# Kernel tuning notes

Measured on AMD Instinct MI355X. Metric: run time of the kernel, lower is better.

Reference implementation:

```python
import jax, jax.numpy as jnp
import numpy as np
from jax import lax


def grouped_linear(x, w):
    # x: [d0, d1, G*ws], w: [G, ws, out_per_group] -> [d0, d1, G*out_per_group]
    d0, d1, _ = x.shape
    G, ws, o = w.shape
    x = x.reshape(d0, d1, G, ws)
    return jnp.einsum('btgi,gio->btgh'.replace('h', 'o'), x, w).reshape(d0, d1, G * o)


def gru_layer(x, w_ih, w_hh, b_ih, b_hh):
    # x: [T, H_in]; w_ih/w_hh: [3, H, H_in]; b_ih/b_hh: [3, H]; gate order (r, z, n)
    ih = jnp.einsum('ti,ghi->tgh', x, w_ih) + b_ih  # input projections for all t at once

    def step(h, ih_t):
        hh = jnp.einsum('i,ghi->gh', h, w_hh) + b_hh
        r = jax.nn.sigmoid(ih_t[0] + hh[0])
        z = jax.nn.sigmoid(ih_t[1] + hh[1])
        n = jnp.tanh(ih_t[2] + r * hh[2])
        h_new = n + z * (h - n)
        return h_new, h_new

    h0 = jnp.zeros((w_hh.shape[1],), x.dtype)
    _, ys = lax.scan(step, h0, ih)
    return ys  # [T, H]


def setup_inputs() -> dict:
    key = jax.random.key(0)
    T, B, H = 8192, 1, 512
    HID, G, L = 512, 8, 2
    C_IN, C_OUT, F, KT = 64, 10, 96, 2
    ks = jax.random.split(key, 17)
    s = jnp.float32(0.05)
    return {
        'emb_tbh': jax.random.normal(ks[0], (T, B, H), jnp.float32),
        'c0': jax.random.normal(ks[1], (B, C_IN, T, F), jnp.float32),
        'lin_in_w': jax.random.normal(ks[2], (G, H // G, HID // G), jnp.float32) * s,
        'gru_w_ih': jax.random.normal(ks[3], (L, 3, HID, HID), jnp.float32) * s,
        'gru_w_hh': jax.random.normal(ks[4], (L, 3, HID, HID), jnp.float32) * s,
        'gru_b_ih': jax.random.normal(ks[5], (L, 3, HID), jnp.float32) * s,
        'gru_b_hh': jax.random.normal(ks[6], (L, 3, HID), jnp.float32) * s,
        'gru_skip_w': jax.random.normal(ks[7], (HID, HID), jnp.float32) * s,
        'gru_skip_b': jax.random.normal(ks[8], (HID,), jnp.float32) * s,
        'lin_out_w': jax.random.normal(ks[9], (G, HID // G, HID // G), jnp.float32) * s,
        'df_skip_w': jax.random.normal(ks[10], (HID, H), jnp.float32) * s,
        'df_skip_b': jax.random.normal(ks[11], (HID,), jnp.float32) * s,
        'fc_a_w': jax.random.normal(ks[12], (1, HID), jnp.float32) * s,
        'fc_a_b': jax.random.normal(ks[13], (1,), jnp.float32) * s,
        'df_out_w': jax.random.normal(ks[14], (G, HID // G, (F * C_OUT) // G), jnp.float32) * s,
        'convp_w': jax.random.normal(ks[15], (C_OUT, C_IN, KT, 1), jnp.float32) * s,
        'convp_b': jax.random.normal(ks[16], (C_OUT,), jnp.float32) * s,
    }


def reference(emb_tbh, c0, lin_in_w, gru_w_ih, gru_w_hh, gru_b_ih, gru_b_hh,
              gru_skip_w, gru_skip_b, lin_out_w, df_skip_w, df_skip_b,
              fc_a_w, fc_a_b, df_out_w, convp_w, convp_b):
    T, B, H = emb_tbh.shape  # B == 1 (manual GRU loop assumes it)
    DF_BINS, DF_OUT_CH = 96, 10

    # --- squeezed GRU: grouped linear_in + ReLU, manual GRU layers, skip, grouped linear_out + ReLU
    x = jax.nn.relu(grouped_linear(emb_tbh, lin_in_w))  # [T, B, HID]
    gru_in = x
    h = x[:, 0, :]  # [T, HID], B == 1
    for l in range(gru_w_ih.shape[0]):
        h = gru_layer(h, gru_w_ih[l], gru_w_hh[l], gru_b_ih[l], gru_b_hh[l])
    x = h[:, None, :]
    x = x + (gru_in @ gru_skip_w.T + gru_skip_b)
    x = jax.nn.relu(grouped_linear(x, lin_out_w))  # [T, B, HID]

    # --- skip from embedding + alpha head
    emb = emb_tbh.reshape(B, T, H)  # B==1: pure relabel of dims
    c = x.reshape(B, T, -1)
    c = c + (emb @ df_skip_w.T + df_skip_b)
    alpha = jax.nn.sigmoid(c @ fc_a_w.T + fc_a_b)  # [B, T, 1]

    # --- df_convp: causal time pad (top=1) + Conv2d kernel (2,1), then permute to [B,T,F,Cout]
    c0p = jnp.pad(c0, ((0, 0), (0, 0), (1, 0), (0, 0)))
    c0c = lax.conv_general_dilated(c0p, convp_w, (1, 1), 'VALID',
                                   dimension_numbers=('NCHW', 'OIHW', 'NCHW'))
    c0c = c0c + convp_b[None, :, None, None]
    c0c = jnp.transpose(c0c, (0, 2, 3, 1))  # [B, T, F, Cout]

    # --- df_out: grouped linear + tanh, reshape to coef grid, add conv pathway
    c = jnp.tanh(grouped_linear(c, df_out_w))  # [B, T, F*Cout]
    c = c.reshape(B, T, DF_BINS, DF_OUT_CH) + c0c
    return (c, alpha)
```

## Files before the change

### kernel.cpp

```cpp
#include <hip/hip_runtime.h>
#include <hip/hip_bf16.h>
#include <cstdint>

#define T_STEPS 8192
#define NWG3 64

typedef unsigned long long ull;

__device__ __forceinline__ float sigmoidf_(float v) { return 1.f / (1.f + __expf(-v)); }

__device__ __forceinline__ ull packpair(float v, unsigned tag) {
  return ((ull)__float_as_uint(v) << 32) | (ull)tag;
}

__device__ __forceinline__ void acc4(float& acc, const float4& wv, const float4& hv) {
  acc = fmaf(hv.x, wv.x, acc); acc = fmaf(hv.y, wv.y, acc);
  acc = fmaf(hv.z, wv.z, acc); acc = fmaf(hv.w, wv.w, acc);
}

__global__ __launch_bounds__(256) void k_grouped_relu(const float* __restrict__ in,
                                                      const float* __restrict__ W,
                                                      float* __restrict__ out) {
  __shared__ float es[512];
  const int t = blockIdx.x;
  const int tid = threadIdx.x;
  const float* inr = in + (size_t)t * 512;
  ((float2*)es)[tid] = ((const float2*)inr)[tid];
  __syncthreads();
#pragma unroll
  for (int rep = 0; rep < 2; ++rep) {
    int jj = tid + rep * 256;
    int g = jj >> 6, o = jj & 63;
    const float* wp = W + (g << 12) + o;
    const float* ep = es + (g << 6);
    float acc = 0.f;
#pragma unroll 8
    for (int i = 0; i < 64; ++i) acc = fmaf(ep[i], wp[i << 6], acc);
    out[(size_t)t * 512 + jj] = fmaxf(acc, 0.f);
  }
}

__global__ __launch_bounds__(256) void k_gemm_rr(const float* __restrict__ A,
                                                 const float* __restrict__ B,
                                                 const float* __restrict__ bias,
                                                 const float* __restrict__ add,
                                                 float* __restrict__ C, int N) {
  __shared__ float As[64][68];
  __shared__ float Bs[64][68];
  const int bm = blockIdx.x << 6, bn = blockIdx.y << 6;
  const int tid = threadIdx.x;
  const int tx = tid & 15, ty = tid >> 4;
  float acc[4][4] = {};
  for (int k0 = 0; k0 < 512; k0 += 64) {
#pragma unroll
    for (int u = 0; u < 4; ++u) {
      int f4 = (u << 8) + tid;
      int m = f4 >> 4;
      int kq = (f4 & 15) << 2;
      float4 av = *(const float4*)(A + (size_t)(bm + m) * 512 + k0 + kq);
      As[kq + 0][m] = av.x; As[kq + 1][m] = av.y; As[kq + 2][m] = av.z; As[kq + 3][m] = av.w;
      float4 bv = *(const float4*)(B + (size_t)(bn + m) * 512 + k0 + kq);
      Bs[kq + 0][m] = bv.x; Bs[kq + 1][m] = bv.y; Bs[kq + 2][m] = bv.z; Bs[kq + 3][m] = bv.w;
    }
    __syncthreads();
#pragma unroll
    for (int k = 0; k < 64; ++k) {
      float4 a4 = *(const float4*)(&As[k][ty << 2]);
      float4 b4 = *(const float4*)(&Bs[k][tx << 2]);
      float ar[4] = {a4.x, a4.y, a4.z, a4.w};
      float br[4] = {b4.x, b4.y, b4.z, b4.w};
#pragma unroll
      for (int i = 0; i < 4; ++i)
#pragma unroll
        for (int j = 0; j < 4; ++j) acc[i][j] = fmaf(ar[i], br[j], acc[i][j]);
    }
    __syncthreads();
  }
  const int n0 = bn + (tx << 2);
  float4 bsv = *(const float4*)(bias + n0);
#pragma unroll
  for (int i = 0; i < 4; ++i) {
    int m = bm + (ty << 2) + i;
    float4 res;
    res.x = acc[i][0] + bsv.x; res.y = acc[i][1] + bsv.y;
    res.z = acc[i][2] + bsv.z; res.w = acc[i][3] + bsv.w;
    if (add) {
      float4 ad = *(const float4*)(add + (size_t)m * N + n0);
      res.x += ad.x; res.y += ad.y; res.z += ad.z; res.w += ad.w;
    }
    *(float4*)(C + (size_t)m * N + n0) = res;
  }
}

__global__ __launch_bounds__(512, 1) void k_gru_fused(
    const float* __restrict__ ih0,
    const float* __restrict__ Whh0, const float* __restrict__ bhh0,
    const float* __restrict__ Wih1, const float* __restrict__ bih1,
    const float* __restrict__ Whh1, const float* __restrict__ bhh1,
    float* __restrict__ h1seq,
    ull* ring0,
    ull* ring1) {
  __shared__ float h0s[512];
  __shared__ float h1s[512];
  const int wg = blockIdx.x, tid = threadIdx.x;
  const int w = tid >> 6, l = tid & 63;
  const int r = (wg << 3) + w;
  const bool pollH1 = (w >= 4);
  const int pidx = ((w & 3) << 6) + l;

  float4 W9[9][2];
#pragma unroll
  for (int g = 0; g < 3; ++g) {
    size_t off = ((size_t)g << 18) + ((size_t)r << 9) + ((size_t)l << 3);
    W9[g][0]     = *(const float4*)(Whh0 + off); W9[g][1]     = *(const float4*)(Whh0 + off + 4);
    W9[3 + g][0] = *(const float4*)(Wih1 + off); W9[3 + g][1] = *(const float4*)(Wih1 + off + 4);
    W9[6 + g][0] = *(const float4*)(Whh1 + off); W9[6 + g][1] = *(const float4*)(Whh1 + off + 4);
  }
  float b9[9] = {};
  if (l == 0) {
#pragma unroll
    for (int g = 0; g < 3; ++g) {
      b9[g] = bhh0[(g << 9) + r];
      b9[3 + g] = bih1[(g << 9) + r];
      b9[6 + g] = bhh1[(g << 9) + r];
    }
  }
  float h0own = 0.f, h1own = 0.f;

  for (int t = 0; t <= T_STEPS; ++t) {
    float i0 = 0.f, i1 = 0.f, i2 = 0.f;
    if (l == 0 && t < T_STEPS) {
      const float* p = ih0 + (size_t)t * 1536 + r;
      i0 = p[0]; i1 = p[512]; i2 = p[1024];
    }
    {
      ull* sp = pollH1 ? (ring1 + ((t & 1) << 9)) : (ring0 + (((t + 1) & 1) << 9));
      const unsigned expm = pollH1 ? (unsigned)((t > 0) ? t - 1 : 0) : (unsigned)t;
      ull Pa, Pb;
      for (;;) {
        Pa = __hip_atomic_load(sp + pidx, __ATOMIC_RELAXED, __HIP_MEMORY_SCOPE_AGENT);
        Pb = __hip_atomic_load(sp + pidx + 256, __ATOMIC_RELAXED, __HIP_MEMORY_SCOPE_AGENT);
        bool bad = (((unsigned)Pa) != expm) | (((unsigned)Pb) != expm);
        if (__ballot(bad) == 0ull) break;
      }
      float* dst = pollH1 ? h1s : h0s;
      dst[pidx] = __uint_as_float((unsigned)(Pa >> 32));
      dst[pidx + 256] = __uint_as_float((unsigned)(Pb >> 32));
    }
    __syncthreads();
    float4 h0a = *(const float4*)(h0s + (l << 3));
    float4 h0b = *(const float4*)(h0s + (l << 3) + 4);
    float4 h1a = *(const float4*)(h1s + (l << 3));
    float4 h1b = *(const float4*)(h1s + (l << 3) + 4);
    __syncthreads();
    float acc[9];
#pragma unroll
    for (int i = 0; i < 9; ++i) acc[i] = 0.f;
#pragma unroll
    for (int i = 0; i < 6; ++i) { acc4(acc[i], W9[i][0], h0a); acc4(acc[i], W9[i][1], h0b); }
#pragma unroll
    for (int i = 6; i < 9; ++i) { acc4(acc[i], W9[i][0], h1a); acc4(acc[i], W9[i][1], h1b); }
#pragma unroll
    for (int m = 1; m < 64; m <<= 1)
#pragma unroll
      for (int i = 0; i < 9; ++i) acc[i] += __shfl_xor(acc[i], m);
    if (l == 0) {
      if (t < T_STEPS) {
        float rr = sigmoidf_(i0 + acc[0] + b9[0]);
        float zz = sigmoidf_(i1 + acc[1] + b9[1]);
        float nn = tanhf(fmaf(rr, acc[2] + b9[2], i2));
        h0own = fmaf(zz, h0own - nn, nn);
        __hip_atomic_store(ring0 + ((t & 1) << 9) + r, packpair(h0own, (unsigned)(t + 1)),
                           __ATOMIC_RELAXED, __HIP_MEMORY_SCOPE_AGENT);
      }
      if (t >= 1) {
        float rr = sigmoidf_(acc[3] + b9[3] + acc[6] + b9[6]);
        float zz = sigmoidf_(acc[4] + b9[4] + acc[7] + b9[7]);
        float nn = tanhf(fmaf(rr, acc[8] + b9[8], acc[5] + b9[5]));
        h1own = fmaf(zz, h1own - nn, nn);
        __hip_atomic_store(ring1 + (((t + 1) & 1) << 9) + r, packpair(h1own, (unsigned)t),
                           __ATOMIC_RELAXED, __HIP_MEMORY_SCOPE_AGENT);
        h1seq[(size_t)(t - 1) * 512 + r] = h1own;
      }
    }
  }
}

__global__ __launch_bounds__(256) void k_alpha(const float* __restrict__ c,
                                               const float* __restrict__ w,
                                               const float* __restrict__ b,
                                               float* __restrict__ alpha) {
  const int wave = threadIdx.x >> 6, lane = threadIdx.x & 63;
  const int t = (blockIdx.x << 2) + wave;
  const float* cr = c + (size_t)t * 512;
  float acc = 0.f;
#pragma unroll
  for (int q = 0; q < 8; ++q) acc = fmaf(cr[lane + (q << 6)], w[lane + (q << 6)], acc);
#pragma unroll
  for (int m = 32; m; m >>= 1) acc += __shfl_xor(acc, m);
  if (lane == 0) alpha[t] = sigmoidf_(acc + b[0]);
}

__global__ __launch_bounds__(256) void k_dfout_conv(const float* __restrict__ c,
                                                    const float* __restrict__ Wd,
                                                    const float* __restrict__ c0,
                                                    const float* __restrict__ wc,
                                                    const float* __restrict__ bc,
                                                    float* __restrict__ out) {
  __shared__ float cs[512];
  __shared__ float A0[64 * 96];
  __shared__ float A1[64 * 96];
  __shared__ float wcs[1280];
  __shared__ float cc[960];
  const int t = blockIdx.x, tid = threadIdx.x;
  ((float2*)cs)[tid] = ((const float2*)(c + (size_t)t * 512))[tid];
  for (int idx = tid; idx < 64 * 96; idx += 256) {
    int ci = idx / 96, f = idx - ci * 96;
    size_t base = (size_t)ci * ((size_t)T_STEPS * 96) + (size_t)t * 96 + f;
    A1[idx] = c0[base];
    A0[idx] = (t == 0) ? 0.f : c0[base - 96];
  }
  for (int idx = tid; idx < 1280; idx += 256) wcs[idx] = wc[idx];
  __syncthreads();
  for (int idx = tid; idx < 960; idx += 256) {
    int f = idx / 10, co = idx - f * 10;
    float acc = bc[co];
    const float* w = wcs + (co << 7);
#pragma unroll 16
    for (int ci = 0; ci < 64; ++ci) {
      acc = fmaf(A0[ci * 96 + f], w[ci * 2 + 0], acc);
      acc = fmaf(A1[ci * 96 + f], w[ci * 2 + 1], acc);
    }
    cc[idx] = acc;
  }
  __syncthreads();
  for (int idx = tid; idx < 960; idx += 256) {
    int g = idx / 120, o = idx - g * 120;
    const float* wp = Wd + g * 7680 + o;
    const float* ep = cs + (g << 6);
    float acc = 0.f;
#pragma unroll 16
    for (int i = 0; i < 64; ++i) acc = fmaf(ep[i], wp[i * 120], acc);
    out[(size_t)t * 960 + idx] = tanhf(acc) + cc[idx];
  }
}

extern "C" void kernel_launch(void* const* d_in, const int* in_sizes, int n_in,
                              void* d_out, int out_size, void* d_ws, size_t ws_size,
                              hipStream_t stream) {
  const float* emb       = (const float*)d_in[0];
  const float* c0        = (const float*)d_in[1];
  const float* lin_in_w  = (const float*)d_in[2];
  const float* w_ih      = (const float*)d_in[3];
  const float* w_hh      = (const float*)d_in[4];
  const float* b_ih      = (const float*)d_in[5];
  const float* b_hh      = (const float*)d_in[6];
  const float* skip_w    = (const float*)d_in[7];
  const float* skip_b    = (const float*)d_in[8];
  const float* lin_out_w = (const float*)d_in[9];
  const float* df_skip_w = (const float*)d_in[10];
  const float* df_skip_b = (const float*)d_in[11];
  const float* fc_a_w    = (const float*)d_in[12];
  const float* fc_a_b    = (const float*)d_in[13];
  const float* df_out_w  = (const float*)d_in[14];
  const float* convp_w   = (const float*)d_in[15];
  const float* convp_b   = (const float*)d_in[16];

  const size_t T = T_STEPS;
  float* x    = (float*)d_ws;
  float* ih   = x + T * 512;
  float* h1   = ih + T * 1536;
  ull* ring0  = (ull*)(h1 + T * 512);
  ull* ring1  = ring0 + 1024;
  float* sbuf = ih;
  float* vbuf = ih + T * 512;
  float* cbuf = ih + 2 * T * 512;
  float* outc = (float*)d_out;
  float* outa = outc + T * 960;

  k_grouped_relu<<<T_STEPS, 256, 0, stream>>>(emb, lin_in_w, x);
  k_gemm_rr<<<dim3(128, 24), 256, 0, stream>>>(x, w_ih, b_ih, nullptr, ih, 1536);
  (void)hipMemsetAsync(ring0, 0, 2048 * sizeof(ull), stream);
  k_gru_fused<<<NWG3, 512, 0, stream>>>(ih, w_hh, b_hh,
                                        w_ih + 786432, b_ih + 1536,
                                        w_hh + 786432, b_hh + 1536,
                                        h1, ring0, ring1);
  k_gemm_rr<<<dim3(128, 8), 256, 0, stream>>>(x, skip_w, skip_b, h1, sbuf, 512);
  k_grouped_relu<<<T_STEPS, 256, 0, stream>>>(sbuf, lin_out_w, vbuf);
  k_gemm_rr<<<dim3(128, 8), 256, 0, stream>>>(emb, df_skip_w, df_skip_b, vbuf, cbuf, 512);
  k_alpha<<<T_STEPS / 4, 256, 0, stream>>>(cbuf, fc_a_w, fc_a_b, outa);
  k_dfout_conv<<<T_STEPS, 256, 0, stream>>>(cbuf, df_out_w, c0, convp_w, convp_b, outc);
  (void)in_sizes; (void)n_in; (void)out_size; (void)ws_size;
}
```

Measured before the change: 31.13 ms.

## Double-buffer GRU hidden-state LDS to drop second barrier; use fast sigmoid/tanh

The persistent GRU kernel now keeps two copies of the shared-memory hidden-state buffers, indexed by step parity, so the second __syncthreads per timestep can be removed. It also swaps sigmoid and tanhf for fast-divide and exp-based approximations, and pins the weight registers with empty asm statements to stop the compiler from rematerialising or spilling them. This targets per-step latency on the serial recurrence, at the cost of slightly lower accuracy in the activations and double the LDS use.

```diff
diff --git a/kernel.cpp b/kernel.cpp
--- a/kernel.cpp
+++ b/kernel.cpp
@@ -7,7 +7,12 @@
 
 typedef unsigned long long ull;
 
-__device__ __forceinline__ float sigmoidf_(float v) { return 1.f / (1.f + __expf(-v)); }
+__device__ __forceinline__ float fast_sigmoid(float v) {
+  return __fdividef(1.f, 1.f + __expf(-v));
+}
+__device__ __forceinline__ float fast_tanh(float v) {
+  return 1.f - __fdividef(2.f, __expf(2.f * v) + 1.f);
+}
 
 __device__ __forceinline__ ull packpair(float v, unsigned tag) {
   return ((ull)__float_as_uint(v) << 32) | (ull)tag;
@@ -16,6 +21,10 @@
 __device__ __forceinline__ void acc4(float& acc, const float4& wv, const float4& hv) {
   acc = fmaf(hv.x, wv.x, acc); acc = fmaf(hv.y, wv.y, acc);
   acc = fmaf(hv.z, wv.z, acc); acc = fmaf(hv.w, wv.w, acc);
+}
+
+__device__ __forceinline__ void pin4(float4& v) {
+  asm volatile("" : "+v"(v.x), "+v"(v.y), "+v"(v.z), "+v"(v.w));
 }
 
 __global__ __launch_bounds__(256) void k_grouped_relu(const float* __restrict__ in,
@@ -98,10 +107,10 @@
     const float* __restrict__ Wih1, const float* __restrict__ bih1,
     const float* __restrict__ Whh1, const float* __restrict__ bhh1,
     float* __restrict__ h1seq,
-    ull* ring0,
-    ull* ring1) {
-  __shared__ float h0s[512];
-  __shared__ float h1s[512];
+    ull* __restrict__ ring0,
+    ull* __restrict__ ring1) {
+  __shared__ float h0s[2][512];
+  __shared__ float h1s[2][512];
   const int wg = blockIdx.x, tid = threadIdx.x;
   const int w = tid >> 6, l = tid & 63;
   const int r = (wg << 3) + w;
@@ -116,6 +125,8 @@
     W9[3 + g][0] = *(const float4*)(Wih1 + off); W9[3 + g][1] = *(const float4*)(Wih1 + off + 4);
     W9[6 + g][0] = *(const float4*)(Whh1 + off); W9[6 + g][1] = *(const float4*)(Whh1 + off + 4);
   }
+#pragma unroll
+  for (int i = 0; i < 9; ++i) { pin4(W9[i][0]); pin4(W9[i][1]); }
   float b9[9] = {};
   if (l == 0) {
 #pragma unroll
@@ -125,6 +136,8 @@
       b9[6 + g] = bhh1[(g << 9) + r];
     }
   }
+#pragma unroll
+  for (int i = 0; i < 9; ++i) asm volatile("" : "+v"(b9[i]));
   float h0own = 0.f, h1own = 0.f;
 
   for (int t = 0; t <= T_STEPS; ++t) {
@@ -143,16 +156,15 @@
         bool bad = (((unsigned)Pa) != expm) | (((unsigned)Pb) != expm);
         if (__ballot(bad) == 0ull) break;
       }
-      float* dst = pollH1 ? h1s : h0s;
+      float* dst = pollH1 ? h1s[t & 1] : h0s[t & 1];
       dst[pidx] = __uint_as_float((unsigned)(Pa >> 32));
       dst[pidx + 256] = __uint_as_float((unsigned)(Pb >> 32));
     }
     __syncthreads();
-    float4 h0a = *(const float4*)(h0s + (l << 3));
-    float4 h0b = *(const float4*)(h0s + (l << 3) + 4);
-    float4 h1a = *(const float4*)(h1s + (l << 3));
-    float4 h1b = *(const float4*)(h1s + (l << 3) + 4);
-    __syncthreads();
+    float4 h0a = *(const float4*)(&h0s[t & 1][l << 3]);
+    float4 h0b = *(const float4*)(&h0s[t & 1][(l << 3) + 4]);
+    float4 h1a = *(const float4*)(&h1s[t & 1][l << 3]);
+    float4 h1b = *(const float4*)(&h1s[t & 1][(l << 3) + 4]);
     float acc[9];
 #pragma unroll
     for (int i = 0; i < 9; ++i) acc[i] = 0.f;
@@ -166,17 +178,17 @@
       for (int i = 0; i < 9; ++i) acc[i] += __shfl_xor(acc[i], m);
     if (l == 0) {
       if (t < T_STEPS) {
-        float rr = sigmoidf_(i0 + acc[0] + b9[0]);
-        float zz = sigmoidf_(i1 + acc[1] + b9[1]);
-        float nn = tanhf(fmaf(rr, acc[2] + b9[2], i2));
+        float rr = fast_sigmoid(i0 + acc[0] + b9[0]);
+        float zz = fast_sigmoid(i1 + acc[1] + b9[1]);
+        float nn = fast_tanh(fmaf(rr, acc[2] + b9[2], i2));
         h0own = fmaf(zz, h0own - nn, nn);
         __hip_atomic_store(ring0 + ((t & 1) << 9) + r, packpair(h0own, (unsigned)(t + 1)),
                            __ATOMIC_RELAXED, __HIP_MEMORY_SCOPE_AGENT);
       }
       if (t >= 1) {
-        float rr = sigmoidf_(acc[3] + b9[3] + acc[6] + b9[6]);
-        float zz = sigmoidf_(acc[4] + b9[4] + acc[7] + b9[7]);
-        float nn = tanhf(fmaf(rr, acc[8] + b9[8], acc[5] + b9[5]));
+        float rr = fast_sigmoid(acc[3] + b9[3] + acc[6] + b9[6]);
+        float zz = fast_sigmoid(acc[4] + b9[4] + acc[7] + b9[7]);
+        float nn = fast_tanh(fmaf(rr, acc[8] + b9[8], acc[5] + b9[5]));
         h1own = fmaf(zz, h1own - nn, nn);
         __hip_atomic_store(ring1 + (((t + 1) & 1) << 9) + r, packpair(h1own, (unsigned)t),
                            __ATOMIC_RELAXED, __HIP_MEMORY_SCOPE_AGENT);
@@ -198,7 +210,7 @@
   for (int q = 0; q < 8; ++q) acc = fmaf(cr[lane + (q << 6)], w[lane + (q << 6)], acc);
 #pragma unroll
   for (int m = 32; m; m >>= 1) acc += __shfl_xor(acc, m);
-  if (lane == 0) alpha[t] = sigmoidf_(acc + b[0]);
+  if (lane == 0) alpha[t] = 1.f / (1.f + __expf(-(acc + b[0])));
 }
 
 __global__ __launch_bounds__(256) void k_dfout_conv(const float* __restrict__ c,
```

Measured after the change: 34.67 ms. 11.4% more time.
